# Kernel tuning notes

Hardware: AMD Instinct MI355X
Metric: run time of the kernel (lower is better)

The kernel has to match this reference:

```python
import jax, jax.numpy as jnp
import numpy as np

MAX_LENGTH = 10
SOS = 0
H = 1024
V = 32000
B = 256
S = 64


def setup_inputs() -> dict:
    key = jax.random.key(0)
    ks = jax.random.split(key, 16)
    sc = 1.0 / np.sqrt(H)
    return {
        "encoder_outputs": jax.random.normal(ks[0], (B, S, H), jnp.float32),
        "encoder_hidden": jax.random.normal(ks[1], (1, B, H), jnp.float32),
        "target_tensor": jax.random.randint(ks[2], (B, MAX_LENGTH), 0, V),
        "embedding": jax.random.normal(ks[3], (V, H), jnp.float32),
        "Wa_w": jax.random.uniform(ks[4], (H, H), jnp.float32, -sc, sc),
        "Wa_b": jax.random.uniform(ks[5], (H,), jnp.float32, -sc, sc),
        "Ua_w": jax.random.uniform(ks[6], (H, H), jnp.float32, -sc, sc),
        "Ua_b": jax.random.uniform(ks[7], (H,), jnp.float32, -sc, sc),
        "Va_w": jax.random.uniform(ks[8], (1, H), jnp.float32, -sc, sc),
        "Va_b": jax.random.uniform(ks[9], (1,), jnp.float32, -sc, sc),
        "gru_w_ih": jax.random.uniform(ks[10], (3 * H, 2 * H), jnp.float32, -sc, sc),
        "gru_w_hh": jax.random.uniform(ks[11], (3 * H, H), jnp.float32, -sc, sc),
        "gru_b_ih": jax.random.uniform(ks[12], (3 * H,), jnp.float32, -sc, sc),
        "gru_b_hh": jax.random.uniform(ks[13], (3 * H,), jnp.float32, -sc, sc),
        "out_w": jax.random.uniform(ks[14], (V, H), jnp.float32, -sc, sc),
        "out_b": jax.random.uniform(ks[15], (V,), jnp.float32, -sc, sc),
    }


def reference(encoder_outputs, encoder_hidden, target_tensor, embedding,
              Wa_w, Wa_b, Ua_w, Ua_b, Va_w, Va_b,
              gru_w_ih, gru_w_hh, gru_b_ih, gru_b_hh, out_w, out_b):
    keys = encoder_outputs                      # [B,S,H]
    # Ua(keys) is step-invariant: hoist out of the decode loop.
    Uk = jnp.einsum('bsh,kh->bsk', keys, Ua_w) + Ua_b  # [B,S,H]
    h0 = encoder_hidden[0]                      # [B,H]
    # teacher forcing: input at step i is SOS for i=0 else target[:, i-1]
    toks = jnp.concatenate(
        [jnp.full((B, 1), SOS, dtype=target_tensor.dtype),
         target_tensor[:, :MAX_LENGTH - 1]], axis=1).T  # [T,B]

    def step(h, tok):
        emb = embedding[tok]                               # [B,H] (dropout = identity in eval)
        wq = jnp.dot(h, Wa_w.T) + Wa_b                     # [B,H]
        e = jnp.tanh(wq[:, None, :] + Uk)                  # [B,S,H]
        scores = jnp.einsum('bsh,h->bs', e, Va_w[0]) + Va_b[0]
        w = jax.nn.softmax(scores, axis=-1)                # [B,S]
        ctx = jnp.einsum('bs,bsh->bh', w, keys)            # [B,H]
        x = jnp.concatenate([emb, ctx], axis=-1)           # [B,2H]
        gi = jnp.dot(x, gru_w_ih.T) + gru_b_ih             # [B,3H]
        gh = jnp.dot(h, gru_w_hh.T) + gru_b_hh             # [B,3H]
        ir, iz, inn = jnp.split(gi, 3, axis=-1)
        hr, hz, hn = jnp.split(gh, 3, axis=-1)
        r = jax.nn.sigmoid(ir + hr)
        z = jax.nn.sigmoid(iz + hz)
        n = jnp.tanh(inn + r * hn)
        h2 = (1.0 - z) * n + z * h                         # [B,H]
        logits = jnp.dot(h2, out_w.T) + out_b              # [B,V]
        return h2, (logits, w)

    h_last, (logits, attn) = jax.lax.scan(step, h0, toks)
    dec_out = jax.nn.log_softmax(jnp.transpose(logits, (1, 0, 2)), axis=-1)  # [B,T,V]
    attentions = jnp.transpose(attn, (1, 0, 2))            # [B,T,S]
    return dec_out, h_last[None, :, :], attentions
```

## Files before the change

### kernel.cpp

```cpp
#include <hip/hip_runtime.h>
#include <math.h>

#define H 1024
#define V 32000
#define B 256
#define S 64
#define T 10

#define GBK 32

typedef __attribute__((ext_vector_type(8))) short bf16x8;
typedef __attribute__((ext_vector_type(4))) float f32x4;

static __device__ __forceinline__ unsigned short f2bf(float f) {
  unsigned int u = __float_as_uint(f);
  u += 0x7fff + ((u >> 16) & 1);
  return (unsigned short)(u >> 16);
}
static __device__ __forceinline__ float bf2f(unsigned short u) {
  return __uint_as_float(((unsigned int)u) << 16);
}
static __device__ __forceinline__ float fast_tanh(float x) {
  float e = __expf(2.f * x);
  return 1.f - 2.f * __builtin_amdgcn_rcpf(e + 1.f);
}
static __device__ __forceinline__ float fast_sigmoid(float x) {
  return __builtin_amdgcn_rcpf(1.f + __expf(-x));
}

static __device__ __forceinline__ void load_lds16(const void* g, void* l) {
  __builtin_amdgcn_global_load_lds(
      (const __attribute__((address_space(1))) unsigned int*)g,
      (__attribute__((address_space(3))) unsigned int*)l, 16, 0, 0);
}

static __device__ __forceinline__ int lds_off(int row, int g) {
  return row * GBK + ((g ^ ((row >> 1) & 3)) * 8);
}

template <int TM, int TN, int MODE, int GRIDMODE, int STAGES>
__global__ __launch_bounds__(256) void gemm_mfma(
    const unsigned short* __restrict__ A, const unsigned short* __restrict__ W,
    const float* __restrict__ aux, float* __restrict__ C,
    unsigned short* __restrict__ Cb,
    int M, int N, int K, int ldc) {
  constexpr int FM = TM / 32;
  constexpr int FN = TN / 32;
  constexpr int CA = TM / 64;
  constexpr int CB = TN / 64;
  constexpr int LOADS = CA + CB;
  constexpr int F = (STAGES >= 3) ? (STAGES - 2) : 0;

  __shared__ unsigned short lsA[STAGES][TM * GBK];
  __shared__ unsigned short lsB[STAGES][TN * GBK];
  const int tid = threadIdx.x;
  const int lane = tid & 63;
  const int w = tid >> 6;

  int mIdx, nIdx;
  if constexpr (GRIDMODE == 1) {
    const int nwg = gridDim.x * gridDim.y;
    const int orig = blockIdx.y * gridDim.x + blockIdx.x;
    const int q = nwg >> 3, rr = nwg & 7;
    const int xcd = orig & 7, rest = orig >> 3;
    const int wgid =
        (xcd < rr ? xcd * (q + 1) : rr * (q + 1) + (xcd - rr) * q) + rest;
    mIdx = wgid % gridDim.x;
    nIdx = wgid / gridDim.x;
  } else {
    mIdx = blockIdx.y;
    nIdx = blockIdx.x;
  }
  const int mBase = mIdx * TM;
  const int nBase = nIdx * TN;
  const int rowBase = (w >> 1) * (TM / 2);
  const int colBase = (w & 1) * (TN / 2);

  const int fr = lane & 15;
  const int fkU = lane >> 4;
  const int fg = lane >> 4;

  f32x4 acc[FM][FN] = {};

  auto STAGE = [&](int buf, int k0) {
#pragma unroll
    for (int i = 0; i < CA; ++i) {
      int chunk = i * 256 + tid;
      int row = chunk >> 2;
      int u = chunk & 3;
      int col = (u ^ ((row >> 1) & 3)) * 8;
      load_lds16(A + (size_t)(mBase + row) * K + k0 + col,
                 &lsA[buf][chunk * 8]);
    }
#pragma unroll
    for (int i = 0; i < CB; ++i) {
      int chunk = i * 256 + tid;
      int row = chunk >> 2;
      int u = chunk & 3;
      int col = (u ^ ((row >> 1) & 3)) * 8;
      load_lds16(W + (size_t)(nBase + row) * K + k0 + col,
                 &lsB[buf][chunk * 8]);
    }
  };

  const int NT = K / GBK;
  for (int s = 0; s <= F && s < NT; ++s) STAGE(s % STAGES, s * GBK);

  for (int t = 0; t < NT; ++t) {
    const int rem = NT - 1 - t;
    if (rem >= F) {
      asm volatile("s_waitcnt vmcnt(%0)\n\ts_barrier" :: "i"(F * LOADS)
                   : "memory");
    } else if (rem == 2) {
      asm volatile("s_waitcnt vmcnt(%0)\n\ts_barrier" :: "i"(2 * LOADS)
                   : "memory");
    } else if (rem == 1) {
      asm volatile("s_waitcnt vmcnt(%0)\n\ts_barrier" :: "i"(1 * LOADS)
                   : "memory");
    } else {
      asm volatile("s_waitcnt vmcnt(0)\n\ts_barrier" ::: "memory");
    }
    if (t + F + 1 < NT) STAGE((t + F + 1) % STAGES, (t + F + 1) * GBK);

    const int cb = t % STAGES;
    bf16x8 af[FM], bfr[FN];
#pragma unroll
    for (int m = 0; m < FM; ++m)
      af[m] = *(const bf16x8*)&lsA[cb][lds_off(rowBase + m * 16 + fr, fkU)];
#pragma unroll
    for (int n = 0; n < FN; ++n)
      bfr[n] = *(const bf16x8*)&lsB[cb][lds_off(colBase + n * 16 + fr, fkU)];
#pragma unroll
    for (int m = 0; m < FM; ++m)
#pragma unroll
      for (int n = 0; n < FN; ++n)
        acc[m][n] = __builtin_amdgcn_mfma_f32_16x16x32_bf16(
            af[m], bfr[n], acc[m][n], 0, 0, 0);
  }

#pragma unroll
  for (int m = 0; m < FM; ++m) {
    int colg[FN];
    float bv[FN];
#pragma unroll
    for (int n = 0; n < FN; ++n) {
      colg[n] = nBase + colBase + n * 16 + fr;
      if constexpr (MODE != 2) bv[n] = aux[colg[n]];
    }
#pragma unroll
    for (int r = 0; r < 4; ++r) {
      const int rowg = mBase + rowBase + m * 16 + fg * 4 + r;
      float v[FN];
#pragma unroll
      for (int n = 0; n < FN; ++n) {
        if constexpr (MODE == 2)
          v[n] = acc[m][n][r] + aux[(size_t)rowg * ldc + colg[n]];
        else
          v[n] = acc[m][n][r] + bv[n];
        if constexpr (MODE == 1)
          Cb[(size_t)rowg * ldc + colg[n]] = f2bf(v[n]);
        else
          C[(size_t)rowg * ldc + colg[n]] = v[n];
      }
    }
  }
}

__global__ __launch_bounds__(256) void gemm_fp8_logits(
    const unsigned char* __restrict__ A8, const unsigned char* __restrict__ W8,
    const float* __restrict__ bias, unsigned short* __restrict__ Cb,
    float* __restrict__ partials, int M, int N, int K, int ldc, int pstride) {
  constexpr int BK = 64;
  __shared__ __align__(16) unsigned char lsA[2][128 * BK];
  __shared__ __align__(16) unsigned char lsB[2][128 * BK];
  const int tid = threadIdx.x;
  const int lane = tid & 63;
  const int w = tid >> 6;

  const int nwg = gridDim.x * gridDim.y;
  const int orig = blockIdx.y * gridDim.x + blockIdx.x;
  const int q = nwg >> 3, rr = nwg & 7;
  const int xcd = orig & 7, rest = orig >> 3;
  const int wgid =
      (xcd < rr ? xcd * (q + 1) : rr * (q + 1) + (xcd - rr) * q) + rest;
  const int mIdx = wgid % gridDim.x;
  const int nIdx = wgid / gridDim.x;
  const int mBase = mIdx * 128;
  const int nBase = nIdx * 128;
  const int rowBase = (w >> 1) * 64;
  const int colBase = (w & 1) * 64;
  const int fr = lane & 15;
  const int fkU = lane >> 4;
  const int fg = lane >> 4;

  f32x4 acc[4][4] = {};

  auto STAGE = [&](int buf, int k0) {
#pragma unroll
    for (int i = 0; i < 2; ++i) {
      int c = i * 256 + tid;
      int row = c >> 2;
      int u = c & 3;
      int col = (u ^ ((row >> 1) & 3)) * 16;
      load_lds16(A8 + (size_t)(mBase + row) * K + k0 + col, &lsA[buf][c * 16]);
    }
#pragma unroll
    for (int i = 0; i < 2; ++i) {
      int c = i * 256 + tid;
      int row = c >> 2;
      int u = c & 3;
      int col = (u ^ ((row >> 1) & 3)) * 16;
      load_lds16(W8 + (size_t)(nBase + row) * K + k0 + col, &lsB[buf][c * 16]);
    }
  };

  const int NT = K / BK;
  STAGE(0, 0);
  int cb = 0;
  for (int t = 0; t < NT; ++t) {
    asm volatile("s_waitcnt vmcnt(0)\n\ts_barrier" ::: "memory");
    if (t + 1 < NT) STAGE(cb ^ 1, (t + 1) * BK);
#pragma unroll
    for (int ks = 0; ks < 2; ++ks) {
      const int u = ks * 2 + (fkU >> 1);
      const int sub = (fkU & 1) * 8;
      long long af[4], bf[4];
#pragma unroll
      for (int m = 0; m < 4; ++m) {
        int row = rowBase + m * 16 + fr;
        af[m] = *(const long long*)
            &lsA[cb][row * BK + ((u ^ ((row >> 1) & 3)) << 4) + sub];
      }
#pragma unroll
      for (int n = 0; n < 4; ++n) {
        int row = colBase + n * 16 + fr;
        bf[n] = *(const long long*)
            &lsB[cb][row * BK + ((u ^ ((row >> 1) & 3)) << 4) + sub];
      }
#pragma unroll
      for (int m = 0; m < 4; ++m)
#pragma unroll
        for (int n = 0; n < 4; ++n)
          acc[m][n] = __builtin_amdgcn_mfma_f32_16x16x32_fp8_fp8(
              af[m], bf[n], acc[m][n], 0, 0, 0);
    }
    cb ^= 1;
  }

#pragma unroll
  for (int m = 0; m < 4; ++m) {
    int colg[4];
    float bv[4];
#pragma unroll
    for (int n = 0; n < 4; ++n) {
      colg[n] = nBase + colBase + n * 16 + fr;
      bv[n] = bias[colg[n]];
    }
#pragma unroll
    for (int r = 0; r < 4; ++r) {
      const int rowg = mBase + rowBase + m * 16 + fg * 4 + r;
      float v[4];
#pragma unroll
      for (int n = 0; n < 4; ++n) {
        v[n] = acc[m][n][r] + bv[n];
        Cb[(size_t)rowg * ldc + colg[n]] = f2bf(v[n]);
      }
      float mx = fmaxf(fmaxf(v[0], v[1]), fmaxf(v[2], v[3]));
      mx = fmaxf(mx, __shfl_xor(mx, 1, 64));
      mx = fmaxf(mx, __shfl_xor(mx, 2, 64));
      mx = fmaxf(mx, __shfl_xor(mx, 4, 64));
      mx = fmaxf(mx, __shfl_xor(mx, 8, 64));
      float se = __expf(v[0] - mx) + __expf(v[1] - mx) +
                 __expf(v[2] - mx) + __expf(v[3] - mx);
      se += __shfl_xor(se, 1, 64);
      se += __shfl_xor(se, 2, 64);
      se += __shfl_xor(se, 4, 64);
      se += __shfl_xor(se, 8, 64);
      if (fr == 0) {
        float2* pp = (float2*)partials;
        pp[(size_t)rowg * pstride + nIdx * 2 + (w & 1)] = make_float2(mx, se);
      }
    }
  }
}

__global__ __launch_bounds__(256) void cvt_bf16_kernel(
    const float* __restrict__ src, unsigned short* __restrict__ dst) {
  size_t i = ((size_t)blockIdx.x * 256 + threadIdx.x) * 8;
  float4 a = *(const float4*)&src[i];
  float4 b = *(const float4*)&src[i + 4];
  ushort4 lo, hi;
  lo.x = f2bf(a.x); lo.y = f2bf(a.y); lo.z = f2bf(a.z); lo.w = f2bf(a.w);
  hi.x = f2bf(b.x); hi.y = f2bf(b.y); hi.z = f2bf(b.z); hi.w = f2bf(b.w);
  *(ushort4*)&dst[i] = lo;
  *(ushort4*)&dst[i + 4] = hi;
}

__global__ __launch_bounds__(256) void cvt_fp8_kernel(
    const float* __restrict__ src, unsigned int* __restrict__ dst) {
  size_t i = (size_t)blockIdx.x * 256 + threadIdx.x;
  float4 a = ((const float4*)src)[i * 2];
  float4 b = ((const float4*)src)[i * 2 + 1];
  int lo = __builtin_amdgcn_cvt_pk_fp8_f32(a.x, a.y, 0, false);
  lo = __builtin_amdgcn_cvt_pk_fp8_f32(a.z, a.w, lo, true);
  int hi = __builtin_amdgcn_cvt_pk_fp8_f32(b.x, b.y, 0, false);
  hi = __builtin_amdgcn_cvt_pk_fp8_f32(b.z, b.w, hi, true);
  ((int2*)dst)[i] = make_int2(lo, hi);
}

__global__ __launch_bounds__(256) void cvt_split_wih(
    const float* __restrict__ w_ih, unsigned short* __restrict__ Wemb,
    unsigned short* __restrict__ Wctx) {
  size_t base = ((size_t)blockIdx.x * 256 + threadIdx.x) * 8;
  int row = (int)(base >> 11);
  int col = (int)(base & 2047);
  float4 a = *(const float4*)&w_ih[base];
  float4 b = *(const float4*)&w_ih[base + 4];
  ushort4 lo, hi;
  lo.x = f2bf(a.x); lo.y = f2bf(a.y); lo.z = f2bf(a.z); lo.w = f2bf(a.w);
  hi.x = f2bf(b.x); hi.y = f2bf(b.y); hi.z = f2bf(b.z); hi.w = f2bf(b.w);
  unsigned short* dst = (col < H) ? (Wemb + (size_t)row * H + col)
                                  : (Wctx + (size_t)row * H + col - H);
  *(ushort4*)dst = lo;
  *(ushort4*)(dst + 4) = hi;
}

__global__ __launch_bounds__(256) void build_fused_bias(
    const float* __restrict__ Wa_b, const float* __restrict__ b_hh,
    float* __restrict__ fb) {
  int i = blockIdx.x * 256 + threadIdx.x;
  fb[i] = (i < H) ? Wa_b[i] : b_hh[i - H];
}

__global__ __launch_bounds__(256) void embed_all_kernel(
    const int* __restrict__ target, const float* __restrict__ emb,
    unsigned short* __restrict__ embAll) {
  int idx = blockIdx.x * 256 + threadIdx.x;
  int h8 = (idx & 127) * 8;
  int tb = idx >> 7;
  int t = tb >> 8;
  int b = tb & 255;
  int tok = (t == 0) ? 0 : target[b * T + (t - 1)];
  const float* e = emb + (size_t)tok * H + h8;
  float4 a = *(const float4*)e;
  float4 c = *(const float4*)(e + 4);
  ushort4 lo, hi;
  lo.x = f2bf(a.x); lo.y = f2bf(a.y); lo.z = f2bf(a.z); lo.w = f2bf(a.w);
  hi.x = f2bf(c.x); hi.y = f2bf(c.y); hi.z = f2bf(c.z); hi.w = f2bf(c.w);
  unsigned short* d = embAll + (size_t)tb * H + h8;
  *(ushort4*)d = lo;
  *(ushort4*)(d + 4) = hi;
}

__global__ __launch_bounds__(256) void attn_fused_kernel(
    const float* __restrict__ wqgh, const unsigned short* __restrict__ Uk_bf,
    const unsigned short* __restrict__ keys_bf,
    const float* __restrict__ Va_w, const float* __restrict__ Va_b,
    float* __restrict__ out_attn, unsigned short* __restrict__ ctx_bf, int t) {
  const int b = blockIdx.x;
  const int tid = threadIdx.x;
  __shared__ float wqs[H];
  __shared__ float vas[H];
  __shared__ float sw[S];

  ((float4*)wqs)[tid] = ((const float4*)(wqgh + (size_t)b * 4 * H))[tid];
  ((float4*)vas)[tid] = ((const float4*)Va_w)[tid];
  __syncthreads();

  const int s = tid >> 2;
  const int hc = (tid & 3) * 256;
  const unsigned short* uk = Uk_bf + ((size_t)b * S + s) * H + hc;
  float sum = 0.f;
#pragma unroll 4
  for (int i = 0; i < 256; i += 8) {
    bf16x8 u = *(const bf16x8*)&uk[i];
#pragma unroll
    for (int j = 0; j < 8; ++j) {
      float e = fast_tanh(wqs[hc + i + j] + bf2f((unsigned short)u[j]));
      sum += e * vas[hc + i + j];
    }
  }
  sum += __shfl_xor(sum, 1, 64);
  sum += __shfl_xor(sum, 2, 64);
  if ((tid & 3) == 0) sw[s] = sum + Va_b[0];
  __syncthreads();

  if (tid < 64) {
    float v = sw[tid];
    float m = v;
    for (int off = 32; off > 0; off >>= 1) m = fmaxf(m, __shfl_xor(m, off, 64));
    float e = __expf(v - m);
    float sm = e;
    for (int off = 32; off > 0; off >>= 1) sm += __shfl_xor(sm, off, 64);
    float wv = e / sm;
    sw[tid] = wv;
    out_attn[((size_t)b * T + t) * S + tid] = wv;
  }
  __syncthreads();

  const unsigned short* kb = keys_bf + (size_t)b * S * H + tid * 4;
  float c0 = 0.f, c1 = 0.f, c2 = 0.f, c3 = 0.f;
#pragma unroll 8
  for (int s2 = 0; s2 < S; ++s2) {
    float wv = sw[s2];
    ushort4 kv = *(const ushort4*)&kb[(size_t)s2 * H];
    c0 += wv * bf2f(kv.x);
    c1 += wv * bf2f(kv.y);
    c2 += wv * bf2f(kv.z);
    c3 += wv * bf2f(kv.w);
  }
  ushort4 o;
  o.x = f2bf(c0); o.y = f2bf(c1); o.z = f2bf(c2); o.w = f2bf(c3);
  *(ushort4*)&ctx_bf[(size_t)b * H + tid * 4] = o;
}

__global__ __launch_bounds__(256) void gru_kernel(
    const float* __restrict__ gi, const float* __restrict__ wqgh,
    const float* __restrict__ h_in, float* __restrict__ h_out,
    unsigned short* __restrict__ h_out_bf, unsigned int* __restrict__ h_out_f8) {
  int idx = (blockIdx.x * 256 + threadIdx.x) * 4;
  int b = idx >> 10;
  int j = idx & (H - 1);
  const float* gib = gi + (size_t)b * 3 * H;
  const float* ghb = wqgh + (size_t)b * 4 * H + H;
  float4 gr4 = *(const float4*)&gib[j];
  float4 gz4 = *(const float4*)&gib[H + j];
  float4 gn4 = *(const float4*)&gib[2 * H + j];
  float4 hr4 = *(const float4*)&ghb[j];
  float4 hz4 = *(const float4*)&ghb[H + j];
  float4 hn4 = *(const float4*)&ghb[2 * H + j];
  float4 hp4 = *(const float4*)&h_in[idx];
  float4 ho4;
  {
    float r0 = fast_sigmoid(gr4.x + hr4.x);
    float z0 = fast_sigmoid(gz4.x + hz4.x);
    float n0 = fast_tanh(gn4.x + r0 * hn4.x);
    ho4.x = (1.f - z0) * n0 + z0 * hp4.x;
    float r1 = fast_sigmoid(gr4.y + hr4.y);
    float z1 = fast_sigmoid(gz4.y + hz4.y);
    float n1 = fast_tanh(gn4.y + r1 * hn4.y);
    ho4.y = (1.f - z1) * n1 + z1 * hp4.y;
    float r2 = fast_sigmoid(gr4.z + hr4.z);
    float z2 = fast_sigmoid(gz4.z + hz4.z);
    float n2 = fast_tanh(gn4.z + r2 * hn4.z);
    ho4.z = (1.f - z2) * n2 + z2 * hp4.z;
    float r3 = fast_sigmoid(gr4.w + hr4.w);
    float z3 = fast_sigmoid(gz4.w + hz4.w);
    float n3 = fast_tanh(gn4.w + r3 * hn4.w);
    ho4.w = (1.f - z3) * n3 + z3 * hp4.w;
  }
  ushort4 hb4;
  hb4.x = f2bf(ho4.x); hb4.y = f2bf(ho4.y);
  hb4.z = f2bf(ho4.z); hb4.w = f2bf(ho4.w);
  int p8 = __builtin_amdgcn_cvt_pk_fp8_f32(ho4.x, ho4.y, 0, false);
  p8 = __builtin_amdgcn_cvt_pk_fp8_f32(ho4.z, ho4.w, p8, true);
  *(float4*)&h_out[idx] = ho4;
  *(ushort4*)&h_out_bf[idx] = hb4;
  h_out_f8[idx >> 2] = (unsigned int)p8;
}

__global__ __launch_bounds__(256) void logsm_reduce_kernel(
    const float* __restrict__ partials, float* __restrict__ ls, int P) {
  const int row = blockIdx.x;
  const int tid = threadIdx.x;
  const float2* pp = (const float2*)partials + (size_t)row * P;
  __shared__ float red[256];
  float mx = -INFINITY;
  for (int i = tid; i < P; i += 256) mx = fmaxf(mx, pp[i].x);
  red[tid] = mx;
  __syncthreads();
  for (int off = 128; off > 0; off >>= 1) {
    if (tid < off) red[tid] = fmaxf(red[tid], red[tid + off]);
    __syncthreads();
  }
  mx = red[0];
  __syncthreads();
  float sm = 0.f;
  for (int i = tid; i < P; i += 256) sm += pp[i].y * __expf(pp[i].x - mx);
  red[tid] = sm;
  __syncthreads();
  for (int off = 128; off > 0; off >>= 1) {
    if (tid < off) red[tid] += red[tid + off];
    __syncthreads();
  }
  if (tid == 0) ls[row] = mx + __logf(red[0]);
}

__global__ __launch_bounds__(256) void logsm_sub_kernel(
    const unsigned short* __restrict__ logits_bf, const float* __restrict__ ls,
    float* __restrict__ dec) {
  const int tb = blockIdx.y;
  const int t = tb >> 8;
  const int b = tb & 255;
  const int i8 = (blockIdx.x * 256 + threadIdx.x) * 8;
  if (i8 < V) {
    float l = ls[tb];
    const unsigned short* src = logits_bf + (size_t)tb * V + i8;
    bf16x8 u = *(const bf16x8*)src;
    float* d = dec + (size_t)b * T * V + (size_t)t * V + i8;
    float4 o0, o1;
    o0.x = bf2f((unsigned short)u[0]) - l; o0.y = bf2f((unsigned short)u[1]) - l;
    o0.z = bf2f((unsigned short)u[2]) - l; o0.w = bf2f((unsigned short)u[3]) - l;
    o1.x = bf2f((unsigned short)u[4]) - l; o1.y = bf2f((unsigned short)u[5]) - l;
    o1.z = bf2f((unsigned short)u[6]) - l; o1.w = bf2f((unsigned short)u[7]) - l;
    *(float4*)d = o0;
    *(float4*)(d + 4) = o1;
  }
}

__global__ __launch_bounds__(256) void copy_kernel(
    const float* __restrict__ src, float* __restrict__ dst, int n) {
  int i = blockIdx.x * 256 + threadIdx.x;
  if (i < n) dst[i] = src[i];
}

extern "C" void kernel_launch(void* const* d_in, const int* in_sizes, int n_in,
                              void* d_out, int out_size, void* d_ws, size_t ws_size,
                              hipStream_t stream) {
  const float* keys       = (const float*)d_in[0];
  const float* enc_hidden = (const float*)d_in[1];
  const int*   target     = (const int*)d_in[2];
  const float* embedding  = (const float*)d_in[3];
  const float* Wa_w = (const float*)d_in[4];
  const float* Wa_b = (const float*)d_in[5];
  const float* Ua_w = (const float*)d_in[6];
  const float* Ua_b = (const float*)d_in[7];
  const float* Va_w = (const float*)d_in[8];
  const float* Va_b = (const float*)d_in[9];
  const float* gru_w_ih = (const float*)d_in[10];
  const float* gru_w_hh = (const float*)d_in[11];
  const float* gru_b_ih = (const float*)d_in[12];
  const float* gru_b_hh = (const float*)d_in[13];
  const float* out_w = (const float*)d_in[14];
  const float* out_b = (const float*)d_in[15];

  float* out = (float*)d_out;
  float* out_dec  = out;
  float* out_h    = out + (size_t)B * T * V;
  float* out_attn = out + (size_t)B * T * V + (size_t)B * H;

  char* p = (char*)d_ws;
  unsigned short* keys_bf = (unsigned short*)p; p += (size_t)B * S * H * 2;
  unsigned char*  outw8   = (unsigned char*)p;  p += (size_t)V * H;
  unsigned short* Uaw_bf  = (unsigned short*)p; p += (size_t)H * H * 2;
  unsigned short* fusedW  = (unsigned short*)p; p += (size_t)4 * H * H * 2;
  float*          fusedB  = (float*)p;          p += (size_t)4 * H * 4;
  unsigned short* Wemb_bf = (unsigned short*)p; p += (size_t)3 * H * H * 2;
  unsigned short* Wctx_bf = (unsigned short*)p; p += (size_t)3 * H * H * 2;
  unsigned short* embAll  = (unsigned short*)p; p += (size_t)T * B * H * 2;
  unsigned short* Uk_bf   = (unsigned short*)p; p += (size_t)B * S * H * 2;
  float*          giE     = (float*)p;          p += (size_t)T * B * 3 * H * 4;
  float*          wqgh    = (float*)p;          p += (size_t)B * 4 * H * 4;
  unsigned short* ctx_bf  = (unsigned short*)p; p += (size_t)B * H * 2;
  float*          gi      = (float*)p;          p += (size_t)B * 3 * H * 4;
  float*          hA      = (float*)p;          p += (size_t)B * H * 4;
  float*          hB      = (float*)p;          p += (size_t)B * H * 4;
  unsigned short* hAll    = (unsigned short*)p; p += (size_t)(T + 1) * B * H * 2;
  unsigned char*  hAll8   = (unsigned char*)p;  p += (size_t)T * B * H;
  unsigned short* logits_bf = (unsigned short*)p; p += (size_t)T * B * V * 2;
  float*          parts   = (float*)p;          p += (size_t)T * B * 500 * 2 * 4;
  float*          ls      = (float*)p;          p += (size_t)T * B * 4;

  cvt_bf16_kernel<<<(B * S * H) / 2048, 256, 0, stream>>>(keys, keys_bf);
  cvt_fp8_kernel<<<((size_t)V * H) / 2048, 256, 0, stream>>>(
      out_w, (unsigned int*)outw8);
  cvt_bf16_kernel<<<(H * H) / 2048, 256, 0, stream>>>(Ua_w, Uaw_bf);
  cvt_bf16_kernel<<<(H * H) / 2048, 256, 0, stream>>>(Wa_w, fusedW);
  cvt_bf16_kernel<<<(3 * H * H) / 2048, 256, 0, stream>>>(gru_w_hh,
                                                          fusedW + (size_t)H * H);
  build_fused_bias<<<(4 * H) / 256, 256, 0, stream>>>(Wa_b, gru_b_hh, fusedB);
  cvt_split_wih<<<(3 * H * 2 * H) / 2048, 256, 0, stream>>>(gru_w_ih, Wemb_bf,
                                                            Wctx_bf);
  embed_all_kernel<<<(T * B * H / 8) / 256, 256, 0, stream>>>(target, embedding,
                                                              embAll);
  cvt_bf16_kernel<<<(B * H) / 2048, 256, 0, stream>>>(enc_hidden, hAll);

  gemm_mfma<128, 128, 1, 0, 2>
      <<<dim3(H / 128, (B * S) / 128), 256, 0, stream>>>(
          keys_bf, Uaw_bf, Ua_b, nullptr, Uk_bf, B * S, H, H, H);
  gemm_mfma<128, 128, 0, 1, 2>
      <<<dim3((T * B) / 128, 3 * H / 128), 256, 0, stream>>>(
          embAll, Wemb_bf, gru_b_ih, giE, nullptr, T * B, 3 * H, H, 3 * H);

  const float* h_in = enc_hidden;
  float* hbufs[2] = {hA, hB};

  for (int t = 0; t < T; ++t) {
    const unsigned short* hbf_in = hAll + (size_t)t * B * H;
    unsigned short* hbf_out = hAll + (size_t)(t + 1) * B * H;
    unsigned int* h8_out = (unsigned int*)(hAll8 + (size_t)t * B * H);
    float* h_out = hbufs[t & 1];

    gemm_mfma<64, 64, 0, 1, 5><<<dim3(B / 64, 4 * H / 64), 256, 0, stream>>>(
        hbf_in, fusedW, fusedB, wqgh, nullptr, B, 4 * H, H, 4 * H);
    attn_fused_kernel<<<B, 256, 0, stream>>>(
        wqgh, Uk_bf, keys_bf, Va_w, Va_b, out_attn, ctx_bf, t);
    gemm_mfma<64, 64, 2, 1, 5><<<dim3(B / 64, 3 * H / 64), 256, 0, stream>>>(
        ctx_bf, Wctx_bf, giE + (size_t)t * B * 3 * H, gi, nullptr,
        B, 3 * H, H, 3 * H);
    gru_kernel<<<(B * H / 4) / 256, 256, 0, stream>>>(gi, wqgh, h_in, h_out,
                                                      hbf_out, h8_out);

    h_in = h_out;
  }

  gemm_fp8_logits<<<dim3((T * B) / 128, V / 128), 256, 0, stream>>>(
      hAll8, outw8, out_b, logits_bf, parts, T * B, V, H, V, 500);
  logsm_reduce_kernel<<<T * B, 256, 0, stream>>>(parts, ls, 500);
  logsm_sub_kernel<<<dim3((V + 2047) / 2048, T * B), 256, 0, stream>>>(
      logits_bf, ls, out_dec);

  copy_kernel<<<(B * H + 255) / 256, 256, 0, stream>>>(h_in, out_h, B * H);
}
```

Before: 942.4 us.

## Fuse context GEMM with GRU gate update into a single gate-interleaved kernel

Replaces the per-step context-projection GEMM and the separate GRU elementwise kernel with one kernel. Each block computes the r, z and n gate columns for the same 32 hidden units, so the GRU update runs in the epilogue without writing and re-reading the gi buffer, and one launch per decode step is dropped. The new kernel uses a 3-stage LDS pipeline with 64x96 tiles. Its epilogue does scattered scalar stores (including byte-wide fp8 stores) rather than the vectorized stores of the old GRU kernel.

```diff
diff --git a/kernel.cpp b/kernel.cpp
--- a/kernel.cpp
+++ b/kernel.cpp
@@ -162,6 +162,104 @@
         else
           C[(size_t)rowg * ldc + colg[n]] = v[n];
       }
+    }
+  }
+}
+
+__global__ __launch_bounds__(256) void gemm_gru3(
+    const unsigned short* __restrict__ A,
+    const unsigned short* __restrict__ W3,
+    const float* __restrict__ giE_t,
+    const float* __restrict__ wqgh,
+    const float* __restrict__ h_in,
+    float* __restrict__ h_out,
+    unsigned short* __restrict__ h_out_bf,
+    unsigned char* __restrict__ h_out_f8) {
+  constexpr int BK = 64;
+  constexpr int STAGES = 3;
+  constexpr int LOADS = 5;
+  __shared__ unsigned short lsA[STAGES][64 * BK];
+  __shared__ unsigned short lsW[STAGES][96 * BK];
+  const int tid = threadIdx.x;
+  const int lane = tid & 63;
+  const int w = tid >> 6;
+  const int mBase = blockIdx.x * 64;
+  const int jBase = blockIdx.y * 32;
+  const int fr = lane & 15;
+  const int fkU = lane >> 4;
+  const int fg = lane >> 4;
+
+  f32x4 acc[6] = {};
+
+  auto STAGE = [&](int buf, int k0) {
+#pragma unroll
+    for (int i = 0; i < 2; ++i) {
+      int c = i * 256 + tid;
+      int row = c >> 3, u = c & 7;
+      int col = (u ^ (row & 7)) * 8;
+      load_lds16(A + (size_t)(mBase + row) * H + k0 + col, &lsA[buf][c * 8]);
+    }
+#pragma unroll
+    for (int i = 0; i < 3; ++i) {
+      int c = i * 256 + tid;
+      int wr = c >> 3, u = c & 7;
+      int gate = wr >> 5, jj = wr & 31;
+      int col = (u ^ (wr & 7)) * 8;
+      load_lds16(W3 + (size_t)(gate * H + jBase + jj) * H + k0 + col,
+                 &lsW[buf][c * 8]);
+    }
+  };
+
+  const int NT = H / BK;
+  STAGE(0, 0);
+  STAGE(1, BK);
+  for (int t = 0; t < NT; ++t) {
+    const int rem = NT - 1 - t;
+    if (rem >= 1) {
+      asm volatile("s_waitcnt vmcnt(%0)\n\ts_barrier" :: "i"(LOADS)
+                   : "memory");
+    } else {
+      asm volatile("s_waitcnt vmcnt(0)\n\ts_barrier" ::: "memory");
+    }
+    if (t + 2 < NT) STAGE((t + 2) % STAGES, (t + 2) * BK);
+    const int cb = t % STAGES;
+    const int arow = w * 16 + fr;
+#pragma unroll
+    for (int ks = 0; ks < 2; ++ks) {
+      const int u = ks * 4 + fkU;
+      bf16x8 af =
+          *(const bf16x8*)&lsA[cb][arow * BK + ((u ^ (arow & 7)) * 8)];
+#pragma unroll
+      for (int n = 0; n < 6; ++n) {
+        int wr = n * 16 + fr;
+        bf16x8 bf =
+            *(const bf16x8*)&lsW[cb][wr * BK + ((u ^ (wr & 7)) * 8)];
+        acc[n] = __builtin_amdgcn_mfma_f32_16x16x32_bf16(af, bf, acc[n],
+                                                         0, 0, 0);
+      }
+    }
+  }
+
+#pragma unroll
+  for (int r = 0; r < 4; ++r) {
+    const int b = mBase + w * 16 + fg * 4 + r;
+    const float* giE_row = giE_t + (size_t)b * 3 * H;
+    const float* gh_row = wqgh + (size_t)b * 4 * H + H;
+#pragma unroll
+    for (int jjg = 0; jjg < 2; ++jjg) {
+      const int col = jBase + jjg * 16 + fr;
+      float gr = acc[0 + jjg][r] + giE_row[col];
+      float gz = acc[2 + jjg][r] + giE_row[H + col];
+      float gn = acc[4 + jjg][r] + giE_row[2 * H + col];
+      float rr = fast_sigmoid(gr + gh_row[col]);
+      float zz = fast_sigmoid(gz + gh_row[H + col]);
+      float nn = fast_tanh(gn + rr * gh_row[2 * H + col]);
+      float hp = h_in[(size_t)b * H + col];
+      float ho = (1.f - zz) * nn + zz * hp;
+      h_out[(size_t)b * H + col] = ho;
+      h_out_bf[(size_t)b * H + col] = f2bf(ho);
+      int p8 = __builtin_amdgcn_cvt_pk_fp8_f32(ho, ho, 0, false);
+      h_out_f8[(size_t)b * H + col] = (unsigned char)(p8 & 0xff);
     }
   }
 }
@@ -414,51 +512,6 @@
   *(ushort4*)&ctx_bf[(size_t)b * H + tid * 4] = o;
 }
 
-__global__ __launch_bounds__(256) void gru_kernel(
-    const float* __restrict__ gi, const float* __restrict__ wqgh,
-    const float* __restrict__ h_in, float* __restrict__ h_out,
-    unsigned short* __restrict__ h_out_bf, unsigned int* __restrict__ h_out_f8) {
-  int idx = (blockIdx.x * 256 + threadIdx.x) * 4;
-  int b = idx >> 10;
-  int j = idx & (H - 1);
-  const float* gib = gi + (size_t)b * 3 * H;
-  const float* ghb = wqgh + (size_t)b * 4 * H + H;
-  float4 gr4 = *(const float4*)&gib[j];
-  float4 gz4 = *(const float4*)&gib[H + j];
-  float4 gn4 = *(const float4*)&gib[2 * H + j];
-  float4 hr4 = *(const float4*)&ghb[j];
-  float4 hz4 = *(const float4*)&ghb[H + j];
-  float4 hn4 = *(const float4*)&ghb[2 * H + j];
-  float4 hp4 = *(const float4*)&h_in[idx];
-  float4 ho4;
-  {
-    float r0 = fast_sigmoid(gr4.x + hr4.x);
-    float z0 = fast_sigmoid(gz4.x + hz4.x);
-    float n0 = fast_tanh(gn4.x + r0 * hn4.x);
-    ho4.x = (1.f - z0) * n0 + z0 * hp4.x;
-    float r1 = fast_sigmoid(gr4.y + hr4.y);
-    float z1 = fast_sigmoid(gz4.y + hz4.y);
-    float n1 = fast_tanh(gn4.y + r1 * hn4.y);
-    ho4.y = (1.f - z1) * n1 + z1 * hp4.y;
-    float r2 = fast_sigmoid(gr4.z + hr4.z);
-    float z2 = fast_sigmoid(gz4.z + hz4.z);
-    float n2 = fast_tanh(gn4.z + r2 * hn4.z);
-    ho4.z = (1.f - z2) * n2 + z2 * hp4.z;
-    float r3 = fast_sigmoid(gr4.w + hr4.w);
-    float z3 = fast_sigmoid(gz4.w + hz4.w);
-    float n3 = fast_tanh(gn4.w + r3 * hn4.w);
-    ho4.w = (1.f - z3) * n3 + z3 * hp4.w;
-  }
-  ushort4 hb4;
-  hb4.x = f2bf(ho4.x); hb4.y = f2bf(ho4.y);
-  hb4.z = f2bf(ho4.z); hb4.w = f2bf(ho4.w);
-  int p8 = __builtin_amdgcn_cvt_pk_fp8_f32(ho4.x, ho4.y, 0, false);
-  p8 = __builtin_amdgcn_cvt_pk_fp8_f32(ho4.z, ho4.w, p8, true);
-  *(float4*)&h_out[idx] = ho4;
-  *(ushort4*)&h_out_bf[idx] = hb4;
-  h_out_f8[idx >> 2] = (unsigned int)p8;
-}
-
 __global__ __launch_bounds__(256) void logsm_reduce_kernel(
     const float* __restrict__ partials, float* __restrict__ ls, int P) {
   const int row = blockIdx.x;
@@ -552,7 +605,6 @@
   float*          giE     = (float*)p;          p += (size_t)T * B * 3 * H * 4;
   float*          wqgh    = (float*)p;          p += (size_t)B * 4 * H * 4;
   unsigned short* ctx_bf  = (unsigned short*)p; p += (size_t)B * H * 2;
-  float*          gi      = (float*)p;          p += (size_t)B * 3 * H * 4;
   float*          hA      = (float*)p;          p += (size_t)B * H * 4;
   float*          hB      = (float*)p;          p += (size_t)B * H * 4;
   unsigned short* hAll    = (unsigned short*)p; p += (size_t)(T + 1) * B * H * 2;
@@ -588,18 +640,16 @@
   for (int t = 0; t < T; ++t) {
     const unsigned short* hbf_in = hAll + (size_t)t * B * H;
     unsigned short* hbf_out = hAll + (size_t)(t + 1) * B * H;
-    unsigned int* h8_out = (unsigned int*)(hAll8 + (size_t)t * B * H);
+    unsigned char* h8_out = hAll8 + (size_t)t * B * H;
     float* h_out = hbufs[t & 1];
 
     gemm_mfma<64, 64, 0, 1, 5><<<dim3(B / 64, 4 * H / 64), 256, 0, stream>>>(
         hbf_in, fusedW, fusedB, wqgh, nullptr, B, 4 * H, H, 4 * H);
     attn_fused_kernel<<<B, 256, 0, stream>>>(
         wqgh, Uk_bf, keys_bf, Va_w, Va_b, out_attn, ctx_bf, t);
-    gemm_mfma<64, 64, 2, 1, 5><<<dim3(B / 64, 3 * H / 64), 256, 0, stream>>>(
-        ctx_bf, Wctx_bf, giE + (size_t)t * B * 3 * H, gi, nullptr,
-        B, 3 * H, H, 3 * H);
-    gru_kernel<<<(B * H / 4) / 256, 256, 0, stream>>>(gi, wqgh, h_in, h_out,
-                                                      hbf_out, h8_out);
+    gemm_gru3<<<dim3(B / 64, H / 32), 256, 0, stream>>>(
+        ctx_bf, Wctx_bf, giE + (size_t)t * B * 3 * H, wqgh, h_in, h_out,
+        hbf_out, h8_out);
 
     h_in = h_out;
   }
```

Measured after the change: 941.5 us. No clear change (-0.1%).
